# Performance work log

Hardware: AMD Instinct MI355X
Metric: run time of the kernel (lower is better)

## Reference

```python
import jax, jax.numpy as jnp
import numpy as np

N_NODES = 50000
N_EDGES = 800000
D_IN = 64
D_HID = 64
N_LAYERS = 3


def setup_inputs() -> dict:
    key = jax.random.key(0)
    ks = jax.random.split(key, 3 + 2 * N_LAYERS)
    x = jax.random.normal(ks[0], (N_NODES, D_IN), dtype=jnp.float32)
    edge_index = jax.random.randint(ks[1], (2, N_EDGES), 0, N_NODES, dtype=jnp.int64)
    edge_weight = jax.random.uniform(ks[2], (N_EDGES,), dtype=jnp.float32)
    inp = {"x": x, "edge_index": edge_index, "edge_weight": edge_weight}
    dims = [(D_IN, D_HID)] + [(D_HID, D_HID)] * (N_LAYERS - 1)
    for i, (din, dout) in enumerate(dims):
        # Glorot-style init like PyG GCNConv
        scale = jnp.sqrt(6.0 / (din + dout)).astype(jnp.float32)
        inp[f"W{i}"] = jax.random.uniform(ks[3 + 2 * i], (din, dout), dtype=jnp.float32, minval=-1.0, maxval=1.0) * scale
        inp[f"b{i}"] = jnp.zeros((dout,), dtype=jnp.float32)
    return inp


def _gcn_norm(edge_index, edge_weight, num_nodes, dtype):
    # Add self-loops with weight 1, then symmetric normalization (PyG gcn_norm).
    loop = jnp.arange(num_nodes)
    src = jnp.concatenate([edge_index[0], loop])
    dst = jnp.concatenate([edge_index[1], loop])
    w = jnp.concatenate([edge_weight, jnp.ones((num_nodes,), dtype=dtype)])
    deg = jax.ops.segment_sum(w, dst, num_segments=num_nodes)  # [N]
    dinv = jnp.where(deg > 0, jax.lax.rsqrt(deg), jnp.zeros_like(deg))
    norm = dinv[src] * w * dinv[dst]  # [E+N]
    return src, dst, norm


def reference(x, edge_index, edge_weight, W0, b0, W1, b1, W2, b2):
    N = x.shape[0]
    src, dst, norm = _gcn_norm(edge_index, edge_weight, N, x.dtype)
    for W, b in ((W0, b0), (W1, b1), (W2, b2)):
        h = x @ W                                   # [N, dout] linear first (PyG)
        msg = h[src] * norm[:, None]                # gather + scale per edge
        x = jax.ops.segment_sum(msg, dst, num_segments=N) + b  # scatter-add + bias
        x = jax.nn.relu(x)
    return x
```

## Files before the change

### kernel.cpp

```cpp
#include <hip/hip_runtime.h>

#define NN 50000
#define NE 800000
#define D  64
#define NB 782
#define NBLK 256
#define CHUNK 3125
#define CAP 1536
#define CAPTOT (NB * CAP)

__device__ __forceinline__ float blo(unsigned u) { return __uint_as_float(u << 16); }
__device__ __forceinline__ float bhi(unsigned u) { return __uint_as_float(u & 0xFFFF0000u); }
__device__ __forceinline__ unsigned short f2b(float f) {
    unsigned u = __float_as_uint(f);
    return (unsigned short)((u + 0x7FFFu + ((u >> 16) & 1u)) >> 16);
}

__global__ void k_init(int* __restrict__ cursor) {
    int i = blockIdx.x * blockDim.x + threadIdx.x;
    if (i < NB) cursor[i] = i * CAP;
}

__global__ __launch_bounds__(256) void p12(const int* __restrict__ src,
        const int* __restrict__ dst, const float* __restrict__ w,
        int* __restrict__ cursor, int2* __restrict__ stage) {
    __shared__ unsigned se[CHUNK];
    __shared__ float    sw[CHUNK];
    __shared__ int      lh[NB];
    int t = threadIdx.x;
    for (int i = t; i < NB; i += 256) lh[i] = 0;
    __syncthreads();
    int e0 = blockIdx.x * CHUNK;
    for (int i = t; i < CHUNK; i += 256) {
        int e = e0 + i;
        unsigned d = (unsigned)dst[e];
        unsigned s = (unsigned)src[e];
        float wv = w[e];
        unsigned pk = 0xFFFFFFFFu;
        if (d < NN) {
            pk = (s & 0xFFFFu) | ((d & 63u) << 16) | ((d >> 6) << 22);
            atomicAdd(&lh[d >> 6], 1);
        }
        se[i] = pk;
        sw[i] = wv;
    }
    __syncthreads();
    for (int i = t; i < NB; i += 256) {
        int c = lh[i];
        lh[i] = c ? atomicAdd(&cursor[i], c) : 0;
    }
    __syncthreads();
    for (int i = t; i < CHUNK; i += 256) {
        unsigned pk = se[i];
        if (pk != 0xFFFFFFFFu) {
            int bucket = (int)(pk >> 22);
            int pos = atomicAdd(&lh[bucket], 1);
            if (pos < (bucket + 1) * CAP)
                stage[pos] = make_int2((int)(pk & 0x3FFFFFu), __float_as_int(sw[i]));
        }
    }
}

__global__ __launch_bounds__(256) void p3_sort(const int2* __restrict__ stage,
        const int* __restrict__ cursor, int2* __restrict__ csr,
        int* __restrict__ row_ptr, int* __restrict__ row_deg, float* __restrict__ dinv) {
    __shared__ int   hist[64];
    __shared__ int   cur[64];
    __shared__ float wsum[64];
    int b = blockIdx.x, t = threadIdx.x;
    int g0 = b * CAP, g1 = cursor[b];
    if (t < 64) { hist[t] = 0; wsum[t] = 0.f; }
    __syncthreads();
    for (int j = g0 + t; j < g1; j += 256) {
        int2 pk = stage[j];
        int r = (pk.x >> 16) & 63;
        atomicAdd(&hist[r], 1);
        atomicAdd(&wsum[r], __int_as_float(pk.y));
    }
    __syncthreads();
    if (t == 0) {
        int s = g0;
        for (int r = 0; r < 64; ++r) { cur[r] = s; s += hist[r]; }
    }
    __syncthreads();
    if (t < 64) {
        int n = b * 64 + t;
        if (n < NN) {
            row_ptr[n] = cur[t];
            row_deg[n] = hist[t];
            dinv[n] = rsqrtf(wsum[t] + 1.0f);
        }
    }
    __syncthreads();
    for (int j = g0 + t; j < g1; j += 256) {
        int2 pk = stage[j];
        int r = (pk.x >> 16) & 63;
        int pos = atomicAdd(&cur[r], 1);
        csr[pos] = make_int2(pk.x & 0xFFFF, pk.y);
    }
}

__global__ __launch_bounds__(256) void gemm_pre_kernel(const float* __restrict__ x,
        const float* __restrict__ W, const float* __restrict__ dinv,
        unsigned short* __restrict__ hp) {
    __shared__ float xs[16][64];
    int t = threadIdx.x;
    int base = blockIdx.x * 16;
    for (int idx = t; idx < 16 * 64; idx += 256)
        xs[idx >> 6][idx & 63] = x[(size_t)(base + (idx >> 6)) * 64 + (idx & 63)];
    __syncthreads();
    int col = t & 63, rq = t >> 6;
    float wc[64];
#pragma unroll
    for (int k = 0; k < 64; ++k) wc[k] = W[k * 64 + col];
    float acc0 = 0.f, acc1 = 0.f, acc2 = 0.f, acc3 = 0.f;
#pragma unroll
    for (int k = 0; k < 64; ++k) {
        float wk = wc[k];
        acc0 += xs[rq     ][k] * wk;
        acc1 += xs[rq +  4][k] * wk;
        acc2 += xs[rq +  8][k] * wk;
        acc3 += xs[rq + 12][k] * wk;
    }
    int r = base + rq;
    hp[(size_t)(r     ) * 64 + col] = f2b(dinv[r     ] * acc0);
    hp[(size_t)(r +  4) * 64 + col] = f2b(dinv[r +  4] * acc1);
    hp[(size_t)(r +  8) * 64 + col] = f2b(dinv[r +  8] * acc2);
    hp[(size_t)(r + 12) * 64 + col] = f2b(dinv[r + 12] * acc3);
}

__device__ __forceinline__ float4 gather_row(int n, int fq, int qbase,
        const int* __restrict__ row_ptr, const int* __restrict__ row_deg,
        const int2* __restrict__ csr, const uint2* __restrict__ hp64) {
    int s0 = row_ptr[n], s1 = s0 + row_deg[n];
    uint2 self = hp64[(size_t)n * 16 + fq];
    float ax = blo(self.x), ay = bhi(self.x), az = blo(self.y), aw = bhi(self.y);
    float bx = 0.f, by = 0.f, bz = 0.f, bw = 0.f;
    for (int base = s0; base < s1; base += 16) {
        int j = base + fq;
        int si = 0; float wl = 0.f;
        if (j < s1) {
            int2 pk = csr[j];
            si = pk.x;
            wl = __int_as_float(pk.y);
        }
        int m = s1 - base; if (m > 16) m = 16;
        int jj = 0;
        for (; jj + 4 <= m; jj += 4) {
            int a0 = __shfl(si, qbase + jj + 0); float w0 = __shfl(wl, qbase + jj + 0);
            int a1 = __shfl(si, qbase + jj + 1); float w1 = __shfl(wl, qbase + jj + 1);
            int a2 = __shfl(si, qbase + jj + 2); float w2 = __shfl(wl, qbase + jj + 2);
            int a3 = __shfl(si, qbase + jj + 3); float w3 = __shfl(wl, qbase + jj + 3);
            uint2 u0 = hp64[(size_t)a0 * 16 + fq];
            uint2 u1 = hp64[(size_t)a1 * 16 + fq];
            uint2 u2 = hp64[(size_t)a2 * 16 + fq];
            uint2 u3 = hp64[(size_t)a3 * 16 + fq];
            ax += w0 * blo(u0.x); ay += w0 * bhi(u0.x); az += w0 * blo(u0.y); aw += w0 * bhi(u0.y);
            bx += w1 * blo(u1.x); by += w1 * bhi(u1.x); bz += w1 * blo(u1.y); bw += w1 * bhi(u1.y);
            ax += w2 * blo(u2.x); ay += w2 * bhi(u2.x); az += w2 * blo(u2.y); aw += w2 * bhi(u2.y);
            bx += w3 * blo(u3.x); by += w3 * bhi(u3.x); bz += w3 * blo(u3.y); bw += w3 * bhi(u3.y);
        }
        for (; jj < m; ++jj) {
            int a0 = __shfl(si, qbase + jj); float w0 = __shfl(wl, qbase + jj);
            uint2 u0 = hp64[(size_t)a0 * 16 + fq];
            ax += w0 * blo(u0.x); ay += w0 * bhi(u0.x); az += w0 * blo(u0.y); aw += w0 * bhi(u0.y);
        }
    }
    return make_float4(ax + bx, ay + by, az + bz, aw + bw);
}

__global__ __launch_bounds__(256) void fused_kernel(const int* __restrict__ row_ptr,
        const int* __restrict__ row_deg, const int2* __restrict__ csr,
        const float* __restrict__ dinv, const uint2* __restrict__ hp_cur,
        const float* __restrict__ bias, const float* __restrict__ Wn,
        unsigned short* __restrict__ hp_next) {
    __shared__ float ys[16][64];
    int t = threadIdx.x;
    int lane = t & 63, q = lane >> 4, fq = lane & 15;
    int ni = ((t >> 6) << 2) + q;
    int n = blockIdx.x * 16 + ni;
    float4 g = gather_row(n, fq, q << 4, row_ptr, row_deg, csr, hp_cur);
    float dv = dinv[n];
    float4 bb = ((const float4*)bias)[fq];
    float4 y;
    y.x = fmaxf(dv * g.x + bb.x, 0.f);
    y.y = fmaxf(dv * g.y + bb.y, 0.f);
    y.z = fmaxf(dv * g.z + bb.z, 0.f);
    y.w = fmaxf(dv * g.w + bb.w, 0.f);
    ((float4*)ys[ni])[fq] = y;
    __syncthreads();
    int col = lane, rq = t >> 6;
    float wc[64];
#pragma unroll
    for (int k = 0; k < 64; ++k) wc[k] = Wn[k * 64 + col];
    float a0 = 0.f, a1 = 0.f, a2 = 0.f, a3 = 0.f;
#pragma unroll
    for (int k = 0; k < 64; ++k) {
        float wk = wc[k];
        a0 += ys[rq     ][k] * wk;
        a1 += ys[rq +  4][k] * wk;
        a2 += ys[rq +  8][k] * wk;
        a3 += ys[rq + 12][k] * wk;
    }
    int r = blockIdx.x * 16 + rq;
    hp_next[(size_t)(r     ) * 64 + col] = f2b(dinv[r     ] * a0);
    hp_next[(size_t)(r +  4) * 64 + col] = f2b(dinv[r +  4] * a1);
    hp_next[(size_t)(r +  8) * 64 + col] = f2b(dinv[r +  8] * a2);
    hp_next[(size_t)(r + 12) * 64 + col] = f2b(dinv[r + 12] * a3);
}

__global__ __launch_bounds__(256) void final_kernel(const int* __restrict__ row_ptr,
        const int* __restrict__ row_deg, const int2* __restrict__ csr,
        const float* __restrict__ dinv, const uint2* __restrict__ hp_cur,
        const float* __restrict__ bias, float* __restrict__ out) {
    int t = threadIdx.x;
    int lane = t & 63, q = lane >> 4, fq = lane & 15;
    int n = blockIdx.x * 16 + ((t >> 6) << 2) + q;
    float4 g = gather_row(n, fq, q << 4, row_ptr, row_deg, csr, hp_cur);
    float dv = dinv[n];
    float4 bb = ((const float4*)bias)[fq];
    float4 r;
    r.x = fmaxf(dv * g.x + bb.x, 0.f);
    r.y = fmaxf(dv * g.y + bb.y, 0.f);
    r.z = fmaxf(dv * g.z + bb.z, 0.f);
    r.w = fmaxf(dv * g.w + bb.w, 0.f);
    ((float4*)out)[(size_t)n * 16 + fq] = r;
}

extern "C" void kernel_launch(void* const* d_in, const int* in_sizes, int n_in,
                              void* d_out, int out_size, void* d_ws, size_t ws_size,
                              hipStream_t stream) {
    const float* x  = (const float*)d_in[0];
    const int*   ei = (const int*)d_in[1];
    const float* ew = (const float*)d_in[2];
    const float* W0 = (const float*)d_in[3];
    const float* b0 = (const float*)d_in[4];
    const float* W1 = (const float*)d_in[5];
    const float* b1 = (const float*)d_in[6];
    const float* W2 = (const float*)d_in[7];
    const float* b2 = (const float*)d_in[8];
    float*       out = (float*)d_out;

    const int* src = ei;
    const int* dst = ei + NE;

    int2*  stage   = (int2*)d_ws;
    int2*  csr     = stage + CAPTOT;
    int*   cursor  = (int*)(csr + CAPTOT);
    int*   row_ptr = cursor + NB;
    int*   row_deg = row_ptr + NN;
    float* dinv    = (float*)(row_deg + NN);
    unsigned short* hpA = (unsigned short*)(dinv + NN);
    unsigned short* hpB = hpA + (size_t)NN * 64;

    k_init<<<1, 1024, 0, stream>>>(cursor);
    p12<<<NBLK, 256, 0, stream>>>(src, dst, ew, cursor, stage);
    p3_sort<<<NB, 256, 0, stream>>>(stage, cursor, csr, row_ptr, row_deg, dinv);

    gemm_pre_kernel<<<NN / 16, 256, 0, stream>>>(x, W0, dinv, hpA);
    fused_kernel<<<NN / 16, 256, 0, stream>>>(row_ptr, row_deg, csr, dinv,
            (const uint2*)hpA, b0, W1, hpB);
    fused_kernel<<<NN / 16, 256, 0, stream>>>(row_ptr, row_deg, csr, dinv,
            (const uint2*)hpB, b1, W2, hpA);
    final_kernel<<<NN / 16, 256, 0, stream>>>(row_ptr, row_deg, csr, dinv,
            (const uint2*)hpA, b2, out);
}
```

Before: 200.2 us.

## Group nodes by in-degree via counting-sort permutation for balanced gather

Builds a degree histogram during CSR construction and a new kernel produces a permutation of nodes grouped by in-degree. The fused and final aggregation kernels then process nodes in that order, so each wavefront handles nodes with similar edge counts and loop divergence drops. In exchange it adds a kernel launch, global atomics on 64 bins, and output writes and dinv reads that become scattered rather than contiguous.

```diff
diff --git a/kernel.cpp b/kernel.cpp
--- a/kernel.cpp
+++ b/kernel.cpp
@@ -8,6 +8,7 @@
 #define CHUNK 3125
 #define CAP 1536
 #define CAPTOT (NB * CAP)
+#define NDB 64
 
 __device__ __forceinline__ float blo(unsigned u) { return __uint_as_float(u << 16); }
 __device__ __forceinline__ float bhi(unsigned u) { return __uint_as_float(u & 0xFFFF0000u); }
@@ -16,9 +17,11 @@
     return (unsigned short)((u + 0x7FFFu + ((u >> 16) & 1u)) >> 16);
 }
 
-__global__ void k_init(int* __restrict__ cursor) {
+__global__ void k_init(int* __restrict__ cursor, int* __restrict__ dhist,
+                       int* __restrict__ dcur) {
     int i = blockIdx.x * blockDim.x + threadIdx.x;
     if (i < NB) cursor[i] = i * CAP;
+    if (i < NDB) { dhist[i] = 0; dcur[i] = 0; }
 }
 
 __global__ __launch_bounds__(256) void p12(const int* __restrict__ src,
@@ -63,7 +66,8 @@
 
 __global__ __launch_bounds__(256) void p3_sort(const int2* __restrict__ stage,
         const int* __restrict__ cursor, int2* __restrict__ csr,
-        int* __restrict__ row_ptr, int* __restrict__ row_deg, float* __restrict__ dinv) {
+        int* __restrict__ row_ptr, int* __restrict__ row_deg, float* __restrict__ dinv,
+        int* __restrict__ dhist) {
     __shared__ int   hist[64];
     __shared__ int   cur[64];
     __shared__ float wsum[64];
@@ -89,6 +93,8 @@
             row_ptr[n] = cur[t];
             row_deg[n] = hist[t];
             dinv[n] = rsqrtf(wsum[t] + 1.0f);
+            int dbin = hist[t] < NDB ? hist[t] : NDB - 1;
+            atomicAdd(&dhist[dbin], 1);
         }
     }
     __syncthreads();
@@ -97,6 +103,24 @@
         int r = (pk.x >> 16) & 63;
         int pos = atomicAdd(&cur[r], 1);
         csr[pos] = make_int2(pk.x & 0xFFFF, pk.y);
+    }
+}
+
+__global__ __launch_bounds__(256) void p5_perm(const int* __restrict__ row_deg,
+        const int* __restrict__ dhist, int* __restrict__ dcur, int* __restrict__ perm) {
+    __shared__ int pre[NDB];
+    int t = threadIdx.x;
+    if (t == 0) {
+        int s = 0;
+        for (int b = 0; b < NDB; ++b) { pre[b] = s; s += dhist[b]; }
+    }
+    __syncthreads();
+    int n = blockIdx.x * 256 + t;
+    if (n < NN) {
+        int dg = row_deg[n];
+        int dbin = dg < NDB ? dg : NDB - 1;
+        int pos = pre[dbin] + atomicAdd(&dcur[dbin], 1);
+        perm[pos] = n;
     }
 }
 
@@ -169,18 +193,22 @@
     return make_float4(ax + bx, ay + by, az + bz, aw + bw);
 }
 
-__global__ __launch_bounds__(256) void fused_kernel(const int* __restrict__ row_ptr,
-        const int* __restrict__ row_deg, const int2* __restrict__ csr,
-        const float* __restrict__ dinv, const uint2* __restrict__ hp_cur,
-        const float* __restrict__ bias, const float* __restrict__ Wn,
-        unsigned short* __restrict__ hp_next) {
+__global__ __launch_bounds__(256) void fused_kernel(const int* __restrict__ perm,
+        const int* __restrict__ row_ptr, const int* __restrict__ row_deg,
+        const int2* __restrict__ csr, const float* __restrict__ dinv,
+        const uint2* __restrict__ hp_cur, const float* __restrict__ bias,
+        const float* __restrict__ Wn, unsigned short* __restrict__ hp_next) {
     __shared__ float ys[16][64];
+    __shared__ int   pn16[16];
     int t = threadIdx.x;
     int lane = t & 63, q = lane >> 4, fq = lane & 15;
     int ni = ((t >> 6) << 2) + q;
-    int n = blockIdx.x * 16 + ni;
-    float4 g = gather_row(n, fq, q << 4, row_ptr, row_deg, csr, hp_cur);
-    float dv = dinv[n];
+    int slot = blockIdx.x * 16;
+    if (t < 16) pn16[t] = perm[slot + t];
+    __syncthreads();
+    int pn = pn16[ni];
+    float4 g = gather_row(pn, fq, q << 4, row_ptr, row_deg, csr, hp_cur);
+    float dv = dinv[pn];
     float4 bb = ((const float4*)bias)[fq];
     float4 y;
     y.x = fmaxf(dv * g.x + bb.x, 0.f);
@@ -202,29 +230,31 @@
         a2 += ys[rq +  8][k] * wk;
         a3 += ys[rq + 12][k] * wk;
     }
-    int r = blockIdx.x * 16 + rq;
-    hp_next[(size_t)(r     ) * 64 + col] = f2b(dinv[r     ] * a0);
-    hp_next[(size_t)(r +  4) * 64 + col] = f2b(dinv[r +  4] * a1);
-    hp_next[(size_t)(r +  8) * 64 + col] = f2b(dinv[r +  8] * a2);
-    hp_next[(size_t)(r + 12) * 64 + col] = f2b(dinv[r + 12] * a3);
-}
-
-__global__ __launch_bounds__(256) void final_kernel(const int* __restrict__ row_ptr,
-        const int* __restrict__ row_deg, const int2* __restrict__ csr,
-        const float* __restrict__ dinv, const uint2* __restrict__ hp_cur,
-        const float* __restrict__ bias, float* __restrict__ out) {
+    int r0 = pn16[rq], r1 = pn16[rq + 4], r2 = pn16[rq + 8], r3 = pn16[rq + 12];
+    hp_next[(size_t)r0 * 64 + col] = f2b(dinv[r0] * a0);
+    hp_next[(size_t)r1 * 64 + col] = f2b(dinv[r1] * a1);
+    hp_next[(size_t)r2 * 64 + col] = f2b(dinv[r2] * a2);
+    hp_next[(size_t)r3 * 64 + col] = f2b(dinv[r3] * a3);
+}
+
+__global__ __launch_bounds__(256) void final_kernel(const int* __restrict__ perm,
+        const int* __restrict__ row_ptr, const int* __restrict__ row_deg,
+        const int2* __restrict__ csr, const float* __restrict__ dinv,
+        const uint2* __restrict__ hp_cur, const float* __restrict__ bias,
+        float* __restrict__ out) {
     int t = threadIdx.x;
     int lane = t & 63, q = lane >> 4, fq = lane & 15;
-    int n = blockIdx.x * 16 + ((t >> 6) << 2) + q;
-    float4 g = gather_row(n, fq, q << 4, row_ptr, row_deg, csr, hp_cur);
-    float dv = dinv[n];
+    int slot = blockIdx.x * 16 + ((t >> 6) << 2) + q;
+    int pn = perm[slot];
+    float4 g = gather_row(pn, fq, q << 4, row_ptr, row_deg, csr, hp_cur);
+    float dv = dinv[pn];
     float4 bb = ((const float4*)bias)[fq];
     float4 r;
     r.x = fmaxf(dv * g.x + bb.x, 0.f);
     r.y = fmaxf(dv * g.y + bb.y, 0.f);
     r.z = fmaxf(dv * g.z + bb.z, 0.f);
     r.w = fmaxf(dv * g.w + bb.w, 0.f);
-    ((float4*)out)[(size_t)n * 16 + fq] = r;
+    ((float4*)out)[(size_t)pn * 16 + fq] = r;
 }
 
 extern "C" void kernel_launch(void* const* d_in, const int* in_sizes, int n_in,
@@ -250,18 +280,22 @@
     int*   row_ptr = cursor + NB;
     int*   row_deg = row_ptr + NN;
     float* dinv    = (float*)(row_deg + NN);
-    unsigned short* hpA = (unsigned short*)(dinv + NN);
+    int*   dhist   = (int*)(dinv + NN);
+    int*   dcur    = dhist + NDB;
+    int*   perm    = dcur + NDB;
+    unsigned short* hpA = (unsigned short*)(perm + NN);
     unsigned short* hpB = hpA + (size_t)NN * 64;
 
-    k_init<<<1, 1024, 0, stream>>>(cursor);
+    k_init<<<1, 1024, 0, stream>>>(cursor, dhist, dcur);
     p12<<<NBLK, 256, 0, stream>>>(src, dst, ew, cursor, stage);
-    p3_sort<<<NB, 256, 0, stream>>>(stage, cursor, csr, row_ptr, row_deg, dinv);
+    p3_sort<<<NB, 256, 0, stream>>>(stage, cursor, csr, row_ptr, row_deg, dinv, dhist);
+    p5_perm<<<(NN + 255) / 256, 256, 0, stream>>>(row_deg, dhist, dcur, perm);
 
     gemm_pre_kernel<<<NN / 16, 256, 0, stream>>>(x, W0, dinv, hpA);
-    fused_kernel<<<NN / 16, 256, 0, stream>>>(row_ptr, row_deg, csr, dinv,
+    fused_kernel<<<NN / 16, 256, 0, stream>>>(perm, row_ptr, row_deg, csr, dinv,
             (const uint2*)hpA, b0, W1, hpB);
-    fused_kernel<<<NN / 16, 256, 0, stream>>>(row_ptr, row_deg, csr, dinv,
+    fused_kernel<<<NN / 16, 256, 0, stream>>>(perm, row_ptr, row_deg, csr, dinv,
             (const uint2*)hpB, b1, W2, hpA);
-    final_kernel<<<NN / 16, 256, 0, stream>>>(row_ptr, row_deg, csr, dinv,
+    final_kernel<<<NN / 16, 256, 0, stream>>>(perm, row_ptr, row_deg, csr, dinv,
             (const uint2*)hpA, b2, out);
 }
```

Result: slower. 484.1 us (+141.8%).

## Split feature tables into column halves and unfuse gather from GEMM

Applied to the files above, without the earlier changes.

Stores the bf16 transformed features as two 32-column halves so each gather pass touches a smaller table that fits better in cache. The gather/aggregate work is split into per-half blocks, interleaved so nearby blocks share tiles, and the fused gather+GEMM is broken into separate gather and GEMM kernels with an fp32 intermediate. Nontemporal loads and stores are added for streaming data. The cost is extra kernel launches, a write and reread of the fp32 intermediate, and reading the CSR twice per layer.

```diff
diff --git a/kernel.cpp b/kernel.cpp
--- a/kernel.cpp
+++ b/kernel.cpp
@@ -8,6 +8,7 @@
 #define CHUNK 3125
 #define CAP 1536
 #define CAPTOT (NB * CAP)
+#define NTI 3125
 
 __device__ __forceinline__ float blo(unsigned u) { return __uint_as_float(u << 16); }
 __device__ __forceinline__ float bhi(unsigned u) { return __uint_as_float(u & 0xFFFF0000u); }
@@ -102,12 +103,13 @@
 
 __global__ __launch_bounds__(256) void gemm_pre_kernel(const float* __restrict__ x,
         const float* __restrict__ W, const float* __restrict__ dinv,
-        unsigned short* __restrict__ hp) {
+        unsigned short* __restrict__ hpL, unsigned short* __restrict__ hpH) {
     __shared__ float xs[16][64];
     int t = threadIdx.x;
     int base = blockIdx.x * 16;
     for (int idx = t; idx < 16 * 64; idx += 256)
-        xs[idx >> 6][idx & 63] = x[(size_t)(base + (idx >> 6)) * 64 + (idx & 63)];
+        xs[idx >> 6][idx & 63] =
+            __builtin_nontemporal_load(&x[(size_t)(base + (idx >> 6)) * 64 + (idx & 63)]);
     __syncthreads();
     int col = t & 63, rq = t >> 6;
     float wc[64];
@@ -122,27 +124,82 @@
         acc2 += xs[rq +  8][k] * wk;
         acc3 += xs[rq + 12][k] * wk;
     }
+    unsigned short* hh = (col < 32) ? hpL : hpH;
+    int hc = col & 31;
     int r = base + rq;
-    hp[(size_t)(r     ) * 64 + col] = f2b(dinv[r     ] * acc0);
-    hp[(size_t)(r +  4) * 64 + col] = f2b(dinv[r +  4] * acc1);
-    hp[(size_t)(r +  8) * 64 + col] = f2b(dinv[r +  8] * acc2);
-    hp[(size_t)(r + 12) * 64 + col] = f2b(dinv[r + 12] * acc3);
-}
-
-__device__ __forceinline__ float4 gather_row(int n, int fq, int qbase,
-        const int* __restrict__ row_ptr, const int* __restrict__ row_deg,
-        const int2* __restrict__ csr, const uint2* __restrict__ hp64) {
+    hh[(size_t)(r     ) * 32 + hc] = f2b(dinv[r     ] * acc0);
+    hh[(size_t)(r +  4) * 32 + hc] = f2b(dinv[r +  4] * acc1);
+    hh[(size_t)(r +  8) * 32 + hc] = f2b(dinv[r +  8] * acc2);
+    hh[(size_t)(r + 12) * 32 + hc] = f2b(dinv[r + 12] * acc3);
+}
+
+__global__ __launch_bounds__(256) void gemm_mid_kernel(const float* __restrict__ yL,
+        const float* __restrict__ yH, const float* __restrict__ W,
+        const float* __restrict__ dinv,
+        unsigned short* __restrict__ hpL, unsigned short* __restrict__ hpH) {
+    __shared__ float ys[16][64];
+    int t = threadIdx.x;
+    int base = blockIdx.x * 16;
+    for (int idx = t; idx < 16 * 64; idx += 256) {
+        int row = idx >> 6, c = idx & 63;
+        const float* sp = (c < 32) ? &yL[(size_t)(base + row) * 32 + c]
+                                   : &yH[(size_t)(base + row) * 32 + (c - 32)];
+        ys[row][c] = __builtin_nontemporal_load(sp);
+    }
+    __syncthreads();
+    int col = t & 63, rq = t >> 6;
+    float wc[64];
+#pragma unroll
+    for (int k = 0; k < 64; ++k) wc[k] = W[k * 64 + col];
+    float acc0 = 0.f, acc1 = 0.f, acc2 = 0.f, acc3 = 0.f;
+#pragma unroll
+    for (int k = 0; k < 64; ++k) {
+        float wk = wc[k];
+        acc0 += ys[rq     ][k] * wk;
+        acc1 += ys[rq +  4][k] * wk;
+        acc2 += ys[rq +  8][k] * wk;
+        acc3 += ys[rq + 12][k] * wk;
+    }
+    unsigned short* hh = (col < 32) ? hpL : hpH;
+    int hc = col & 31;
+    int r = base + rq;
+    hh[(size_t)(r     ) * 32 + hc] = f2b(dinv[r     ] * acc0);
+    hh[(size_t)(r +  4) * 32 + hc] = f2b(dinv[r +  4] * acc1);
+    hh[(size_t)(r +  8) * 32 + hc] = f2b(dinv[r +  8] * acc2);
+    hh[(size_t)(r + 12) * 32 + hc] = f2b(dinv[r + 12] * acc3);
+}
+
+__global__ __launch_bounds__(256) void gather_half_kernel(const int* __restrict__ row_ptr,
+        const int* __restrict__ row_deg, const int2* __restrict__ csr,
+        const float* __restrict__ dinv, const unsigned* __restrict__ hpL,
+        const unsigned* __restrict__ hpH, const float* __restrict__ bias,
+        float* __restrict__ outL, float* __restrict__ outH, int orow) {
+    int bid = blockIdx.x;
+    int g = bid >> 3, r7 = bid & 7;
+    int half = r7 >> 2;
+    int tile = g * 4 + (r7 & 3);
+    if (tile >= NTI) return;
+    const unsigned* hp = half ? hpH : hpL;
+    const float2* bb2 = (const float2*)(bias + half * 32);
+    float* ob = half ? outH : outL;
+
+    int t = threadIdx.x;
+    int lane = t & 63, q = lane >> 4, fq = lane & 15;
+    int ni = ((t >> 6) << 2) + q;
+    int n = tile * 16 + ni;
+    int qbase = q << 4;
+
     int s0 = row_ptr[n], s1 = s0 + row_deg[n];
-    uint2 self = hp64[(size_t)n * 16 + fq];
-    float ax = blo(self.x), ay = bhi(self.x), az = blo(self.y), aw = bhi(self.y);
-    float bx = 0.f, by = 0.f, bz = 0.f, bw = 0.f;
+    unsigned self = hp[(size_t)n * 16 + fq];
+    float ax = blo(self), ay = bhi(self);
+    float bx = 0.f, by = 0.f;
     for (int base = s0; base < s1; base += 16) {
         int j = base + fq;
         int si = 0; float wl = 0.f;
         if (j < s1) {
-            int2 pk = csr[j];
-            si = pk.x;
-            wl = __int_as_float(pk.y);
+            long long pv = __builtin_nontemporal_load((const long long*)(csr + j));
+            si = (int)(unsigned)(pv & 0xFFFFFFFFll);
+            wl = __int_as_float((int)(pv >> 32));
         }
         int m = s1 - base; if (m > 16) m = 16;
         int jj = 0;
@@ -151,80 +208,28 @@
             int a1 = __shfl(si, qbase + jj + 1); float w1 = __shfl(wl, qbase + jj + 1);
             int a2 = __shfl(si, qbase + jj + 2); float w2 = __shfl(wl, qbase + jj + 2);
             int a3 = __shfl(si, qbase + jj + 3); float w3 = __shfl(wl, qbase + jj + 3);
-            uint2 u0 = hp64[(size_t)a0 * 16 + fq];
-            uint2 u1 = hp64[(size_t)a1 * 16 + fq];
-            uint2 u2 = hp64[(size_t)a2 * 16 + fq];
-            uint2 u3 = hp64[(size_t)a3 * 16 + fq];
-            ax += w0 * blo(u0.x); ay += w0 * bhi(u0.x); az += w0 * blo(u0.y); aw += w0 * bhi(u0.y);
-            bx += w1 * blo(u1.x); by += w1 * bhi(u1.x); bz += w1 * blo(u1.y); bw += w1 * bhi(u1.y);
-            ax += w2 * blo(u2.x); ay += w2 * bhi(u2.x); az += w2 * blo(u2.y); aw += w2 * bhi(u2.y);
-            bx += w3 * blo(u3.x); by += w3 * bhi(u3.x); bz += w3 * blo(u3.y); bw += w3 * bhi(u3.y);
+            unsigned u0 = hp[(size_t)a0 * 16 + fq];
+            unsigned u1 = hp[(size_t)a1 * 16 + fq];
+            unsigned u2 = hp[(size_t)a2 * 16 + fq];
+            unsigned u3 = hp[(size_t)a3 * 16 + fq];
+            ax += w0 * blo(u0); ay += w0 * bhi(u0);
+            bx += w1 * blo(u1); by += w1 * bhi(u1);
+            ax += w2 * blo(u2); ay += w2 * bhi(u2);
+            bx += w3 * blo(u3); by += w3 * bhi(u3);
         }
         for (; jj < m; ++jj) {
             int a0 = __shfl(si, qbase + jj); float w0 = __shfl(wl, qbase + jj);
-            uint2 u0 = hp64[(size_t)a0 * 16 + fq];
-            ax += w0 * blo(u0.x); ay += w0 * bhi(u0.x); az += w0 * blo(u0.y); aw += w0 * bhi(u0.y);
-        }
-    }
-    return make_float4(ax + bx, ay + by, az + bz, aw + bw);
-}
-
-__global__ __launch_bounds__(256) void fused_kernel(const int* __restrict__ row_ptr,
-        const int* __restrict__ row_deg, const int2* __restrict__ csr,
-        const float* __restrict__ dinv, const uint2* __restrict__ hp_cur,
-        const float* __restrict__ bias, const float* __restrict__ Wn,
-        unsigned short* __restrict__ hp_next) {
-    __shared__ float ys[16][64];
-    int t = threadIdx.x;
-    int lane = t & 63, q = lane >> 4, fq = lane & 15;
-    int ni = ((t >> 6) << 2) + q;
-    int n = blockIdx.x * 16 + ni;
-    float4 g = gather_row(n, fq, q << 4, row_ptr, row_deg, csr, hp_cur);
+            unsigned u0 = hp[(size_t)a0 * 16 + fq];
+            ax += w0 * blo(u0); ay += w0 * bhi(u0);
+        }
+    }
     float dv = dinv[n];
-    float4 bb = ((const float4*)bias)[fq];
-    float4 y;
-    y.x = fmaxf(dv * g.x + bb.x, 0.f);
-    y.y = fmaxf(dv * g.y + bb.y, 0.f);
-    y.z = fmaxf(dv * g.z + bb.z, 0.f);
-    y.w = fmaxf(dv * g.w + bb.w, 0.f);
-    ((float4*)ys[ni])[fq] = y;
-    __syncthreads();
-    int col = lane, rq = t >> 6;
-    float wc[64];
-#pragma unroll
-    for (int k = 0; k < 64; ++k) wc[k] = Wn[k * 64 + col];
-    float a0 = 0.f, a1 = 0.f, a2 = 0.f, a3 = 0.f;
-#pragma unroll
-    for (int k = 0; k < 64; ++k) {
-        float wk = wc[k];
-        a0 += ys[rq     ][k] * wk;
-        a1 += ys[rq +  4][k] * wk;
-        a2 += ys[rq +  8][k] * wk;
-        a3 += ys[rq + 12][k] * wk;
-    }
-    int r = blockIdx.x * 16 + rq;
-    hp_next[(size_t)(r     ) * 64 + col] = f2b(dinv[r     ] * a0);
-    hp_next[(size_t)(r +  4) * 64 + col] = f2b(dinv[r +  4] * a1);
-    hp_next[(size_t)(r +  8) * 64 + col] = f2b(dinv[r +  8] * a2);
-    hp_next[(size_t)(r + 12) * 64 + col] = f2b(dinv[r + 12] * a3);
-}
-
-__global__ __launch_bounds__(256) void final_kernel(const int* __restrict__ row_ptr,
-        const int* __restrict__ row_deg, const int2* __restrict__ csr,
-        const float* __restrict__ dinv, const uint2* __restrict__ hp_cur,
-        const float* __restrict__ bias, float* __restrict__ out) {
-    int t = threadIdx.x;
-    int lane = t & 63, q = lane >> 4, fq = lane & 15;
-    int n = blockIdx.x * 16 + ((t >> 6) << 2) + q;
-    float4 g = gather_row(n, fq, q << 4, row_ptr, row_deg, csr, hp_cur);
-    float dv = dinv[n];
-    float4 bb = ((const float4*)bias)[fq];
-    float4 r;
-    r.x = fmaxf(dv * g.x + bb.x, 0.f);
-    r.y = fmaxf(dv * g.y + bb.y, 0.f);
-    r.z = fmaxf(dv * g.z + bb.z, 0.f);
-    r.w = fmaxf(dv * g.w + bb.w, 0.f);
-    ((float4*)out)[(size_t)n * 16 + fq] = r;
+    float2 bb = bb2[fq];
+    float2 yv;
+    yv.x = fmaxf(dv * (ax + bx) + bb.x, 0.f);
+    yv.y = fmaxf(dv * (ay + by) + bb.y, 0.f);
+    union { float2 f; double d; } u; u.f = yv;
+    __builtin_nontemporal_store(u.d, (double*)((float2*)(ob + (size_t)n * orow) + fq));
 }
 
 extern "C" void kernel_launch(void* const* d_in, const int* in_sizes, int n_in,
@@ -244,24 +249,30 @@
     const int* src = ei;
     const int* dst = ei + NE;
 
-    int2*  stage   = (int2*)d_ws;
-    int2*  csr     = stage + CAPTOT;
-    int*   cursor  = (int*)(csr + CAPTOT);
+    int2*  stage = (int2*)d_ws;
+    int2*  csr   = stage + CAPTOT;
+    float* yL    = (float*)(csr + CAPTOT);
+    float* yH    = yL + (size_t)NN * 32;
+    unsigned short* hpAL = (unsigned short*)(yH + (size_t)NN * 32);
+    unsigned short* hpAH = hpAL + (size_t)NN * 32;
+    unsigned short* hpBL = hpAH + (size_t)NN * 32;
+    unsigned short* hpBH = hpBL + (size_t)NN * 32;
+    int*   cursor  = (int*)(hpBH + (size_t)NN * 32);
     int*   row_ptr = cursor + NB;
     int*   row_deg = row_ptr + NN;
     float* dinv    = (float*)(row_deg + NN);
-    unsigned short* hpA = (unsigned short*)(dinv + NN);
-    unsigned short* hpB = hpA + (size_t)NN * 64;
 
     k_init<<<1, 1024, 0, stream>>>(cursor);
     p12<<<NBLK, 256, 0, stream>>>(src, dst, ew, cursor, stage);
     p3_sort<<<NB, 256, 0, stream>>>(stage, cursor, csr, row_ptr, row_deg, dinv);
 
-    gemm_pre_kernel<<<NN / 16, 256, 0, stream>>>(x, W0, dinv, hpA);
-    fused_kernel<<<NN / 16, 256, 0, stream>>>(row_ptr, row_deg, csr, dinv,
-            (const uint2*)hpA, b0, W1, hpB);
-    fused_kernel<<<NN / 16, 256, 0, stream>>>(row_ptr, row_deg, csr, dinv,
-            (const uint2*)hpB, b1, W2, hpA);
-    final_kernel<<<NN / 16, 256, 0, stream>>>(row_ptr, row_deg, csr, dinv,
-            (const uint2*)hpA, b2, out);
-}
+    gemm_pre_kernel<<<NTI, 256, 0, stream>>>(x, W0, dinv, hpAL, hpAH);
+    gather_half_kernel<<<NB * 8, 256, 0, stream>>>(row_ptr, row_deg, csr, dinv,
+            (const unsigned*)hpAL, (const unsigned*)hpAH, b0, yL, yH, 32);
+    gemm_mid_kernel<<<NTI, 256, 0, stream>>>(yL, yH, W1, dinv, hpBL, hpBH);
+    gather_half_kernel<<<NB * 8, 256, 0, stream>>>(row_ptr, row_deg, csr, dinv,
+            (const unsigned*)hpBL, (const unsigned*)hpBH, b1, yL, yH, 32);
+    gemm_mid_kernel<<<NTI, 256, 0, stream>>>(yL, yH, W2, dinv, hpAL, hpAH);
+    gather_half_kernel<<<NB * 8, 256, 0, stream>>>(row_ptr, row_deg, csr, dinv,
+            (const unsigned*)hpAL, (const unsigned*)hpAH, b2, out, out + 32, 64);
+}
```

Result: slower. 260.7 us (+30.2%).
